# Kernel tuning notes

Hardware: AMD Instinct MI355X
Metric: run time of the kernel (lower is better)

Reference implementation:

```python
import jax, jax.numpy as jnp
import numpy as np

N_NODES = 50000
N_EDGES = 800000
D_IN = 100
HID = 128
N_LAYERS = 3
N_GRAPHS = 64


def setup_inputs() -> dict:
    key = jax.random.key(0)
    ks = jax.random.split(key, 10)
    x = jax.random.normal(ks[0], (N_NODES, D_IN), dtype=jnp.float32)
    edge_index = jax.random.randint(ks[1], (2, N_EDGES), 0, N_NODES, dtype=jnp.int64)
    batch = jnp.sort(jax.random.randint(ks[2], (N_NODES,), 0, N_GRAPHS, dtype=jnp.int64))
    s = 1.0 / np.sqrt(D_IN)
    W_enc = jax.random.uniform(ks[3], (D_IN, HID), jnp.float32, -s, s)
    b_enc = jax.random.uniform(ks[4], (HID,), jnp.float32, -s, s)
    sh = 1.0 / np.sqrt(HID)
    gcn_W = jax.random.uniform(ks[5], (N_LAYERS, HID, HID), jnp.float32, -sh, sh)
    gcn_b = jax.random.uniform(ks[6], (N_LAYERS, HID), jnp.float32, -sh, sh)
    W_reg = jax.random.uniform(ks[7], (HID, 1), jnp.float32, -sh, sh)
    b_reg = jax.random.uniform(ks[8], (1,), jnp.float32, -sh, sh)
    return {"x": x, "edge_index": edge_index, "batch": batch,
            "W_enc": W_enc, "b_enc": b_enc, "gcn_W": gcn_W, "gcn_b": gcn_b,
            "W_reg": W_reg, "b_reg": b_reg}


def reference(x, edge_index, batch, W_enc, b_enc, gcn_W, gcn_b, W_reg, b_reg):
    N = x.shape[0]
    # node encoder
    h = x @ W_enc + b_enc  # [N, HID]
    # GCN normalization with self-loops (edge_weight = 1, PyG gcn_norm)
    loop = jnp.arange(N, dtype=edge_index.dtype)
    src = jnp.concatenate([edge_index[0], loop])  # [E+N]
    dst = jnp.concatenate([edge_index[1], loop])
    deg = jax.ops.segment_sum(jnp.ones_like(src, dtype=h.dtype), dst, num_segments=N)
    dinv = jnp.where(deg > 0, jax.lax.rsqrt(deg), 0.0)
    norm = dinv[src] * dinv[dst]  # [E+N]
    for i in range(N_LAYERS):
        m = (h @ gcn_W[i])[src] * norm[:, None]           # gather + scale messages
        h = jax.ops.segment_sum(m, dst, num_segments=N)   # scatter-add aggregate
        h = jax.nn.relu(h + gcn_b[i])
    # global mean pool over graphs
    sums = jax.ops.segment_sum(h, batch, num_segments=N_GRAPHS)
    cnt = jax.ops.segment_sum(jnp.ones((N,), dtype=h.dtype), batch, num_segments=N_GRAPHS)
    pooled = sums / jnp.maximum(cnt, 1.0)[:, None]        # [N_GRAPHS, HID]
    return pooled @ W_reg + b_reg                         # [N_GRAPHS, 1]
```

## Files before the change

kernel.cpp:

```cpp
#include <hip/hip_runtime.h>
#include <hip/hip_fp16.h>

#define N_NODES 50000
#define N_EDGES 800000
#define D_INN 100
#define HID 128
#define N_GRAPHS 64
#define NBLK ((N_NODES + 255) / 256)
#define POOL_ROWS 128
#define POOL_BLOCKS ((N_NODES + POOL_ROWS - 1) / POOL_ROWS)

__global__ void k_init(int* __restrict__ deg, int* __restrict__ cnt,
                       float* __restrict__ sums) {
    int i = blockIdx.x * 256 + threadIdx.x;
    if (i < N_NODES) { deg[i] = 1; cnt[i] = 0; }
    if (i < N_GRAPHS * HID) sums[i] = 0.f;
}

__global__ void k_deg(const int* __restrict__ dst, int* __restrict__ deg) {
    int e = blockIdx.x * 256 + threadIdx.x;
    if (e < N_EDGES) atomicAdd(&deg[dst[e]], 1);
}

__global__ void k_dinv(const int* __restrict__ deg, float* __restrict__ dinv) {
    int i = blockIdx.x * 256 + threadIdx.x;
    if (i < N_NODES) dinv[i] = rsqrtf((float)deg[i]);
}

__global__ __launch_bounds__(256) void k_scan1(const int* __restrict__ deg,
                                               int* __restrict__ incl,
                                               int* __restrict__ bsums) {
    __shared__ int sm[256];
    int i = blockIdx.x * 256 + threadIdx.x;
    int v = (i < N_NODES) ? deg[i] : 0;
    sm[threadIdx.x] = v;
    __syncthreads();
    for (int off = 1; off < 256; off <<= 1) {
        int t = (threadIdx.x >= off) ? sm[threadIdx.x - off] : 0;
        __syncthreads();
        sm[threadIdx.x] += t;
        __syncthreads();
    }
    if (i < N_NODES) incl[i] = sm[threadIdx.x];
    if (threadIdx.x == 255) bsums[blockIdx.x] = sm[255];
}

__global__ __launch_bounds__(256) void k_scan2(const int* __restrict__ bsums,
                                               int* __restrict__ boff) {
    __shared__ int sm[256];
    int v = (threadIdx.x < NBLK) ? bsums[threadIdx.x] : 0;
    sm[threadIdx.x] = v;
    __syncthreads();
    for (int off = 1; off < 256; off <<= 1) {
        int t = (threadIdx.x >= off) ? sm[threadIdx.x - off] : 0;
        __syncthreads();
        sm[threadIdx.x] += t;
        __syncthreads();
    }
    boff[threadIdx.x] = sm[threadIdx.x] - v;
}

__global__ void k_scan3(const int* __restrict__ incl, const int* __restrict__ boff,
                        int* __restrict__ offsets) {
    int i = blockIdx.x * 256 + threadIdx.x;
    if (i < N_NODES) offsets[i + 1] = incl[i] + boff[blockIdx.x];
    if (i == 0) offsets[0] = 0;
}

__global__ void k_fill(const int* __restrict__ src, const int* __restrict__ dst,
                       const int* __restrict__ offsets, int* __restrict__ cnt,
                       int* __restrict__ csr_src) {
    int e = blockIdx.x * 256 + threadIdx.x;
    if (e < N_EDGES) {
        int s = src[e], d = dst[e];
        int pos = offsets[d] + atomicAdd(&cnt[d], 1);
        csr_src[pos] = s;
    } else if (e < N_EDGES + N_NODES) {
        int i = e - N_EDGES;
        int pos = offsets[i] + atomicAdd(&cnt[i], 1);
        csr_src[pos] = i;
    }
}

template <int K, bool BIAS, bool FOLD>
__global__ __launch_bounds__(256) void k_gemm(const float* __restrict__ in,
                                              const float* __restrict__ W,
                                              const float* __restrict__ bias,
                                              const float* __restrict__ dinv,
                                              void* __restrict__ outp) {
    __shared__ float lw[K * HID];
    __shared__ float lx[32 * K];
    for (int i = threadIdx.x; i < K * HID / 4; i += 256)
        ((float4*)lw)[i] = ((const float4*)W)[i];
    const int cq = threadIdx.x & 31;
    const int rg = threadIdx.x >> 5;
    float4 zero; zero.x = zero.y = zero.z = zero.w = 0.f;
    float4 bv = zero;
    if (BIAS) bv = ((const float4*)bias)[cq];
    const float4* lw4 = (const float4*)lw;
    float* outf = (float*)outp;
    __half* outh = (__half*)outp;
    const int nch = (N_NODES + 31) / 32;
    for (int c = blockIdx.x; c < nch; c += gridDim.x) {
        int r0 = c * 32;
        __syncthreads();
        for (int i = threadIdx.x; i < 32 * K / 4; i += 256) {
            int fi = i * 4;
            int rr = fi / K, kk = fi % K;
            int gr = r0 + rr;
            ((float4*)lx)[i] = (gr < N_NODES) ? *(const float4*)(in + gr * K + kk) : zero;
        }
        __syncthreads();
        float4 a0 = bv, a1 = bv, a2 = bv, a3 = bv;
#pragma unroll 8
        for (int k = 0; k < K; ++k) {
            float4 w = lw4[k * 32 + cq];
            float x0 = lx[(rg +  0) * K + k];
            float x1 = lx[(rg +  8) * K + k];
            float x2 = lx[(rg + 16) * K + k];
            float x3 = lx[(rg + 24) * K + k];
            a0.x = fmaf(x0, w.x, a0.x); a0.y = fmaf(x0, w.y, a0.y);
            a0.z = fmaf(x0, w.z, a0.z); a0.w = fmaf(x0, w.w, a0.w);
            a1.x = fmaf(x1, w.x, a1.x); a1.y = fmaf(x1, w.y, a1.y);
            a1.z = fmaf(x1, w.z, a1.z); a1.w = fmaf(x1, w.w, a1.w);
            a2.x = fmaf(x2, w.x, a2.x); a2.y = fmaf(x2, w.y, a2.y);
            a2.z = fmaf(x2, w.z, a2.z); a2.w = fmaf(x2, w.w, a2.w);
            a3.x = fmaf(x3, w.x, a3.x); a3.y = fmaf(x3, w.y, a3.y);
            a3.z = fmaf(x3, w.z, a3.z); a3.w = fmaf(x3, w.w, a3.w);
        }
        int gr = r0 + rg;
        if (FOLD) {
#pragma unroll
            for (int q = 0; q < 4; ++q) {
                int r = gr + q * 8;
                if (r < N_NODES) {
                    float4 a = (q == 0) ? a0 : (q == 1) ? a1 : (q == 2) ? a2 : a3;
                    float s = dinv[r];
                    ushort4 h;
                    h.x = __half_as_ushort(__float2half(a.x * s));
                    h.y = __half_as_ushort(__float2half(a.y * s));
                    h.z = __half_as_ushort(__float2half(a.z * s));
                    h.w = __half_as_ushort(__float2half(a.w * s));
                    *(ushort4*)(outh + r * HID + cq * 4) = h;
                }
            }
        } else {
            if (gr      < N_NODES) *(float4*)(outf + (gr     ) * HID + cq * 4) = a0;
            if (gr +  8 < N_NODES) *(float4*)(outf + (gr +  8) * HID + cq * 4) = a1;
            if (gr + 16 < N_NODES) *(float4*)(outf + (gr + 16) * HID + cq * 4) = a2;
            if (gr + 24 < N_NODES) *(float4*)(outf + (gr + 24) * HID + cq * 4) = a3;
        }
    }
}

__global__ __launch_bounds__(256) void k_agg(const __half* __restrict__ B,
                                             const int* __restrict__ offsets,
                                             const int* __restrict__ csr_src,
                                             const float* __restrict__ dinv,
                                             const float* __restrict__ bias,
                                             float* __restrict__ A) {
    int node = (blockIdx.x * 256 + threadIdx.x) >> 6;
    int lane = threadIdx.x & 63;
    if (node >= N_NODES) return;
    int beg = offsets[node], end = offsets[node + 1];
    float ax0 = 0.f, ay0 = 0.f, ax1 = 0.f, ay1 = 0.f;
    const __half2* B2 = (const __half2*)B;
    int j = beg;
    while (j < end) {
        int take = end - j; if (take > 64) take = 64;
        int s_l = (lane < take) ? csr_src[j + lane] : 0;
        int t = 0;
        for (; t + 4 <= take; t += 4) {
            int s0 = __shfl(s_l, t + 0), s1 = __shfl(s_l, t + 1);
            int s2 = __shfl(s_l, t + 2), s3 = __shfl(s_l, t + 3);
            __half2 v0 = B2[s0 * 64 + lane];
            __half2 v1 = B2[s1 * 64 + lane];
            __half2 v2 = B2[s2 * 64 + lane];
            __half2 v3 = B2[s3 * 64 + lane];
            float2 f0 = __half22float2(v0);
            float2 f1 = __half22float2(v1);
            float2 f2 = __half22float2(v2);
            float2 f3 = __half22float2(v3);
            ax0 += f0.x; ay0 += f0.y;
            ax1 += f1.x; ay1 += f1.y;
            ax0 += f2.x; ay0 += f2.y;
            ax1 += f3.x; ay1 += f3.y;
        }
        for (; t < take; ++t) {
            int s = __shfl(s_l, t);
            float2 f = __half22float2(B2[s * 64 + lane]);
            ax0 += f.x; ay0 += f.y;
        }
        j += take;
    }
    float dn = dinv[node];
    float2 b = ((const float2*)bias)[lane];
    float2 r;
    r.x = fmaxf(fmaf(dn, ax0 + ax1, b.x), 0.f);
    r.y = fmaxf(fmaf(dn, ay0 + ay1, b.y), 0.f);
    ((float2*)A)[node * 64 + lane] = r;
}

__global__ __launch_bounds__(128) void k_pool_part(const float* __restrict__ A,
                                                   const int* __restrict__ batch,
                                                   float* __restrict__ sums) {
    int base = blockIdx.x * POOL_ROWS;
    if (base >= N_NODES) return;
    int c = threadIdx.x;
    int end = base + POOL_ROWS;
    if (end > N_NODES) end = N_NODES;
    float acc = 0.f;
    int g = batch[base];
    for (int n = base; n < end; ++n) {
        int bg = batch[n];
        if (bg != g) {
            atomicAdd(&sums[g * HID + c], acc);
            acc = 0.f;
            g = bg;
        }
        acc += A[n * HID + c];
    }
    atomicAdd(&sums[g * HID + c], acc);
}

__global__ __launch_bounds__(128) void k_head(const float* __restrict__ sums,
                                              const int* __restrict__ batch,
                                              const float* __restrict__ W_reg,
                                              const float* __restrict__ b_reg,
                                              float* __restrict__ out) {
    int g = blockIdx.x;
    int lo = 0, hi = N_NODES;
    while (lo < hi) { int mid = (lo + hi) >> 1; if (batch[mid] < g) lo = mid + 1; else hi = mid; }
    int start = lo;
    hi = N_NODES;
    while (lo < hi) { int mid = (lo + hi) >> 1; if (batch[mid] < g + 1) lo = mid + 1; else hi = mid; }
    int end = lo;
    float cnt = (float)((end - start) > 0 ? (end - start) : 1);
    float v = (sums[g * HID + threadIdx.x] / cnt) * W_reg[threadIdx.x];
    for (int off = 32; off > 0; off >>= 1) v += __shfl_down(v, off);
    __shared__ float sm[2];
    if ((threadIdx.x & 63) == 0) sm[threadIdx.x >> 6] = v;
    __syncthreads();
    if (threadIdx.x == 0) out[g] = sm[0] + sm[1] + b_reg[0];
}

extern "C" void kernel_launch(void* const* d_in, const int* in_sizes, int n_in,
                              void* d_out, int out_size, void* d_ws, size_t ws_size,
                              hipStream_t stream) {
    const float* x      = (const float*)d_in[0];
    const int*   e_src  = (const int*)d_in[1];
    const int*   e_dst  = e_src + N_EDGES;
    const int*   batch  = (const int*)d_in[2];
    const float* W_enc  = (const float*)d_in[3];
    const float* b_enc  = (const float*)d_in[4];
    const float* gcn_W  = (const float*)d_in[5];
    const float* gcn_b  = (const float*)d_in[6];
    const float* W_reg  = (const float*)d_in[7];
    const float* b_reg  = (const float*)d_in[8];
    float* out = (float*)d_out;

    char* p = (char*)d_ws;
    auto carve = [&](size_t bytes) { char* q = p; p += (bytes + 255) & ~(size_t)255; return q; };
    float*  bufA    = (float*) carve(sizeof(float)  * N_NODES * HID);
    __half* bufB    = (__half*)carve(sizeof(__half) * N_NODES * HID);
    int*    csr_src = (int*)   carve(sizeof(int)    * (N_EDGES + N_NODES));
    int*    deg     = (int*)   carve(sizeof(int)    * N_NODES);
    int*    cnt     = (int*)   carve(sizeof(int)    * N_NODES);
    int*    offsets = (int*)   carve(sizeof(int)    * (N_NODES + 1));
    int*    incl    = (int*)   carve(sizeof(int)    * N_NODES);
    int*    bsums   = (int*)   carve(sizeof(int)    * 256);
    int*    boff    = (int*)   carve(sizeof(int)    * 256);
    float*  dinv    = (float*) carve(sizeof(float)  * N_NODES);
    float*  sums    = (float*) carve(sizeof(float)  * N_GRAPHS * HID);

    k_init<<<NBLK, 256, 0, stream>>>(deg, cnt, sums);
    k_deg<<<(N_EDGES + 255) / 256, 256, 0, stream>>>(e_dst, deg);
    k_dinv<<<NBLK, 256, 0, stream>>>(deg, dinv);
    k_scan1<<<NBLK, 256, 0, stream>>>(deg, incl, bsums);
    k_scan2<<<1, 256, 0, stream>>>(bsums, boff);
    k_scan3<<<NBLK, 256, 0, stream>>>(incl, boff, offsets);
    k_fill<<<(N_EDGES + N_NODES + 255) / 256, 256, 0, stream>>>(
        e_src, e_dst, offsets, cnt, csr_src);

    k_gemm<D_INN, true, false><<<512, 256, 0, stream>>>(x, W_enc, b_enc, nullptr, bufA);
    for (int l = 0; l < 3; ++l) {
        k_gemm<HID, false, true><<<512, 256, 0, stream>>>(
            bufA, gcn_W + l * HID * HID, nullptr, dinv, bufB);
        k_agg<<<(N_NODES * 64 + 255) / 256, 256, 0, stream>>>(
            bufB, offsets, csr_src, dinv, gcn_b + l * HID, bufA);
    }
    k_pool_part<<<POOL_BLOCKS, 128, 0, stream>>>(bufA, batch, sums);
    k_head<<<N_GRAPHS, 128, 0, stream>>>(sums, batch, W_reg, b_reg, out);
}
```

Before: 435.2 us.

## Use MFMA fp16 GEMMs, store activations in half, simplify CSR build

```diff
diff --git a/kernel.cpp b/kernel.cpp
--- a/kernel.cpp
+++ b/kernel.cpp
@@ -10,16 +10,24 @@
 #define POOL_ROWS 128
 #define POOL_BLOCKS ((N_NODES + POOL_ROWS - 1) / POOL_ROWS)
 
-__global__ void k_init(int* __restrict__ deg, int* __restrict__ cnt,
-                       float* __restrict__ sums) {
-    int i = blockIdx.x * 256 + threadIdx.x;
-    if (i < N_NODES) { deg[i] = 1; cnt[i] = 0; }
+typedef _Float16 f16x8 __attribute__((ext_vector_type(8)));
+typedef float f32x4 __attribute__((ext_vector_type(4)));
+
+__global__ void k_init(int* __restrict__ deg, float* __restrict__ sums) {
+    int i = blockIdx.x * 256 + threadIdx.x;
+    if (i < N_NODES) deg[i] = 1;
     if (i < N_GRAPHS * HID) sums[i] = 0.f;
 }
 
 __global__ void k_deg(const int* __restrict__ dst, int* __restrict__ deg) {
-    int e = blockIdx.x * 256 + threadIdx.x;
-    if (e < N_EDGES) atomicAdd(&deg[dst[e]], 1);
+    int t = blockIdx.x * 256 + threadIdx.x;
+    if (t < N_EDGES / 4) {
+        int4 d = ((const int4*)dst)[t];
+        atomicAdd(&deg[d.x], 1);
+        atomicAdd(&deg[d.y], 1);
+        atomicAdd(&deg[d.z], 1);
+        atomicAdd(&deg[d.w], 1);
+    }
 }
 
 __global__ void k_dinv(const int* __restrict__ deg, float* __restrict__ dinv) {
@@ -61,33 +69,46 @@
 }
 
 __global__ void k_scan3(const int* __restrict__ incl, const int* __restrict__ boff,
-                        int* __restrict__ offsets) {
-    int i = blockIdx.x * 256 + threadIdx.x;
-    if (i < N_NODES) offsets[i + 1] = incl[i] + boff[blockIdx.x];
+                        const int* __restrict__ deg, int* __restrict__ offsets,
+                        int* __restrict__ cursor, int* __restrict__ csr_src) {
+    int i = blockIdx.x * 256 + threadIdx.x;
+    if (i < N_NODES) {
+        int off1 = incl[i] + boff[blockIdx.x];
+        offsets[i + 1] = off1;
+        int p0 = off1 - deg[i];
+        csr_src[p0] = i;
+        cursor[i] = p0 + 1;
+    }
     if (i == 0) offsets[0] = 0;
 }
 
 __global__ void k_fill(const int* __restrict__ src, const int* __restrict__ dst,
-                       const int* __restrict__ offsets, int* __restrict__ cnt,
-                       int* __restrict__ csr_src) {
-    int e = blockIdx.x * 256 + threadIdx.x;
-    if (e < N_EDGES) {
-        int s = src[e], d = dst[e];
-        int pos = offsets[d] + atomicAdd(&cnt[d], 1);
-        csr_src[pos] = s;
-    } else if (e < N_EDGES + N_NODES) {
-        int i = e - N_EDGES;
-        int pos = offsets[i] + atomicAdd(&cnt[i], 1);
-        csr_src[pos] = i;
-    }
-}
-
-template <int K, bool BIAS, bool FOLD>
-__global__ __launch_bounds__(256) void k_gemm(const float* __restrict__ in,
-                                              const float* __restrict__ W,
-                                              const float* __restrict__ bias,
-                                              const float* __restrict__ dinv,
-                                              void* __restrict__ outp) {
+                       int* __restrict__ cursor, int* __restrict__ csr_src) {
+    int t = blockIdx.x * 256 + threadIdx.x;
+    if (t < N_EDGES / 2) {
+        int2 s = ((const int2*)src)[t];
+        int2 d = ((const int2*)dst)[t];
+        int p0 = atomicAdd(&cursor[d.x], 1);
+        csr_src[p0] = s.x;
+        int p1 = atomicAdd(&cursor[d.y], 1);
+        csr_src[p1] = s.y;
+    }
+}
+
+__global__ void k_wt(const float* __restrict__ W, __half* __restrict__ Wt) {
+    int i = blockIdx.x * 256 + threadIdx.x;
+    if (i < 3 * HID * HID) {
+        int l = i >> 14, rem = i & 16383;
+        int c = rem >> 7, k = rem & 127;
+        Wt[(l << 14) + c * HID + k] = __float2half(W[(l << 14) + k * HID + c]);
+    }
+}
+
+__global__ __launch_bounds__(256) void k_gemm_enc(const float* __restrict__ in,
+                                                  const float* __restrict__ W,
+                                                  const float* __restrict__ bias,
+                                                  __half* __restrict__ outh) {
+    const int K = D_INN;
     __shared__ float lw[K * HID];
     __shared__ float lx[32 * K];
     for (int i = threadIdx.x; i < K * HID / 4; i += 256)
@@ -95,11 +116,8 @@
     const int cq = threadIdx.x & 31;
     const int rg = threadIdx.x >> 5;
     float4 zero; zero.x = zero.y = zero.z = zero.w = 0.f;
-    float4 bv = zero;
-    if (BIAS) bv = ((const float4*)bias)[cq];
+    float4 bv = ((const float4*)bias)[cq];
     const float4* lw4 = (const float4*)lw;
-    float* outf = (float*)outp;
-    __half* outh = (__half*)outp;
     const int nch = (N_NODES + 31) / 32;
     for (int c = blockIdx.x; c < nch; c += gridDim.x) {
         int r0 = c * 32;
@@ -112,7 +130,7 @@
         }
         __syncthreads();
         float4 a0 = bv, a1 = bv, a2 = bv, a3 = bv;
-#pragma unroll 8
+#pragma unroll 4
         for (int k = 0; k < K; ++k) {
             float4 w = lw4[k * 32 + cq];
             float x0 = lx[(rg +  0) * K + k];
@@ -129,26 +147,61 @@
             a3.z = fmaf(x3, w.z, a3.z); a3.w = fmaf(x3, w.w, a3.w);
         }
         int gr = r0 + rg;
-        if (FOLD) {
 #pragma unroll
-            for (int q = 0; q < 4; ++q) {
-                int r = gr + q * 8;
-                if (r < N_NODES) {
-                    float4 a = (q == 0) ? a0 : (q == 1) ? a1 : (q == 2) ? a2 : a3;
-                    float s = dinv[r];
-                    ushort4 h;
-                    h.x = __half_as_ushort(__float2half(a.x * s));
-                    h.y = __half_as_ushort(__float2half(a.y * s));
-                    h.z = __half_as_ushort(__float2half(a.z * s));
-                    h.w = __half_as_ushort(__float2half(a.w * s));
-                    *(ushort4*)(outh + r * HID + cq * 4) = h;
-                }
+        for (int q = 0; q < 4; ++q) {
+            int r = gr + q * 8;
+            if (r < N_NODES) {
+                float4 a = (q == 0) ? a0 : (q == 1) ? a1 : (q == 2) ? a2 : a3;
+                ushort4 h;
+                h.x = __half_as_ushort(__float2half(a.x));
+                h.y = __half_as_ushort(__float2half(a.y));
+                h.z = __half_as_ushort(__float2half(a.z));
+                h.w = __half_as_ushort(__float2half(a.w));
+                *(ushort4*)(outh + r * HID + cq * 4) = h;
             }
-        } else {
-            if (gr      < N_NODES) *(float4*)(outf + (gr     ) * HID + cq * 4) = a0;
-            if (gr +  8 < N_NODES) *(float4*)(outf + (gr +  8) * HID + cq * 4) = a1;
-            if (gr + 16 < N_NODES) *(float4*)(outf + (gr + 16) * HID + cq * 4) = a2;
-            if (gr + 24 < N_NODES) *(float4*)(outf + (gr + 24) * HID + cq * 4) = a3;
+        }
+    }
+}
+
+__global__ __launch_bounds__(256) void k_gemm_mfma(const _Float16* __restrict__ A,
+                                                   const _Float16* __restrict__ Wt,
+                                                   const float* __restrict__ dinv,
+                                                   _Float16* __restrict__ out) {
+    const int lane = threadIdx.x & 63;
+    const int wave = threadIdx.x >> 6;
+    const int l15  = lane & 15;
+    const int lhi  = lane >> 4;
+    f16x8 bf0[4], bf1[4];
+#pragma unroll
+    for (int ks = 0; ks < 4; ++ks) {
+        int col0 = wave * 32 + l15;
+        int col1 = wave * 32 + 16 + l15;
+        bf0[ks] = *(const f16x8*)(Wt + col0 * HID + ks * 32 + lhi * 8);
+        bf1[ks] = *(const f16x8*)(Wt + col1 * HID + ks * 32 + lhi * 8);
+    }
+    for (int chunk = blockIdx.x; chunk < N_NODES / 16; chunk += gridDim.x) {
+        int row0 = chunk * 16;
+        const _Float16* Ar = A + (row0 + l15) * HID + lhi * 8;
+        f16x8 af0 = *(const f16x8*)(Ar);
+        f16x8 af1 = *(const f16x8*)(Ar + 32);
+        f16x8 af2 = *(const f16x8*)(Ar + 64);
+        f16x8 af3 = *(const f16x8*)(Ar + 96);
+        f32x4 acc0 = {0.f, 0.f, 0.f, 0.f};
+        f32x4 acc1 = {0.f, 0.f, 0.f, 0.f};
+        acc0 = __builtin_amdgcn_mfma_f32_16x16x32_f16(af0, bf0[0], acc0, 0, 0, 0);
+        acc1 = __builtin_amdgcn_mfma_f32_16x16x32_f16(af0, bf1[0], acc1, 0, 0, 0);
+        acc0 = __builtin_amdgcn_mfma_f32_16x16x32_f16(af1, bf0[1], acc0, 0, 0, 0);
+        acc1 = __builtin_amdgcn_mfma_f32_16x16x32_f16(af1, bf1[1], acc1, 0, 0, 0);
+        acc0 = __builtin_amdgcn_mfma_f32_16x16x32_f16(af2, bf0[2], acc0, 0, 0, 0);
+        acc1 = __builtin_amdgcn_mfma_f32_16x16x32_f16(af2, bf1[2], acc1, 0, 0, 0);
+        acc0 = __builtin_amdgcn_mfma_f32_16x16x32_f16(af3, bf0[3], acc0, 0, 0, 0);
+        acc1 = __builtin_amdgcn_mfma_f32_16x16x32_f16(af3, bf1[3], acc1, 0, 0, 0);
+#pragma unroll
+        for (int r = 0; r < 4; ++r) {
+            int row = row0 + lhi * 4 + r;
+            float dr = dinv[row];
+            out[row * HID + wave * 32 + l15]      = (_Float16)(acc0[r] * dr);
+            out[row * HID + wave * 32 + 16 + l15] = (_Float16)(acc1[r] * dr);
         }
     }
 }
@@ -158,7 +211,7 @@
                                              const int* __restrict__ csr_src,
                                              const float* __restrict__ dinv,
                                              const float* __restrict__ bias,
-                                             float* __restrict__ A) {
+                                             __half* __restrict__ A) {
     int node = (blockIdx.x * 256 + threadIdx.x) >> 6;
     int lane = threadIdx.x & 63;
     if (node >= N_NODES) return;
@@ -173,14 +226,10 @@
         for (; t + 4 <= take; t += 4) {
             int s0 = __shfl(s_l, t + 0), s1 = __shfl(s_l, t + 1);
             int s2 = __shfl(s_l, t + 2), s3 = __shfl(s_l, t + 3);
-            __half2 v0 = B2[s0 * 64 + lane];
-            __half2 v1 = B2[s1 * 64 + lane];
-            __half2 v2 = B2[s2 * 64 + lane];
-            __half2 v3 = B2[s3 * 64 + lane];
-            float2 f0 = __half22float2(v0);
-            float2 f1 = __half22float2(v1);
-            float2 f2 = __half22float2(v2);
-            float2 f3 = __half22float2(v3);
+            float2 f0 = __half22float2(B2[s0 * 64 + lane]);
+            float2 f1 = __half22float2(B2[s1 * 64 + lane]);
+            float2 f2 = __half22float2(B2[s2 * 64 + lane]);
+            float2 f3 = __half22float2(B2[s3 * 64 + lane]);
             ax0 += f0.x; ay0 += f0.y;
             ax1 += f1.x; ay1 += f1.y;
             ax0 += f2.x; ay0 += f2.y;
@@ -195,32 +244,35 @@
     }
     float dn = dinv[node];
     float2 b = ((const float2*)bias)[lane];
-    float2 r;
-    r.x = fmaxf(fmaf(dn, ax0 + ax1, b.x), 0.f);
-    r.y = fmaxf(fmaf(dn, ay0 + ay1, b.y), 0.f);
-    ((float2*)A)[node * 64 + lane] = r;
-}
-
-__global__ __launch_bounds__(128) void k_pool_part(const float* __restrict__ A,
-                                                   const int* __restrict__ batch,
-                                                   float* __restrict__ sums) {
+    float rx = fmaxf(fmaf(dn, ax0 + ax1, b.x), 0.f);
+    float ry = fmaxf(fmaf(dn, ay0 + ay1, b.y), 0.f);
+    ((__half2*)A)[node * 64 + lane] = __floats2half2_rn(rx, ry);
+}
+
+__global__ __launch_bounds__(64) void k_pool_part(const __half* __restrict__ A,
+                                                  const int* __restrict__ batch,
+                                                  float* __restrict__ sums) {
     int base = blockIdx.x * POOL_ROWS;
     if (base >= N_NODES) return;
     int c = threadIdx.x;
     int end = base + POOL_ROWS;
     if (end > N_NODES) end = N_NODES;
-    float acc = 0.f;
+    const __half2* A2 = (const __half2*)A;
+    float ax = 0.f, ay = 0.f;
     int g = batch[base];
     for (int n = base; n < end; ++n) {
         int bg = batch[n];
         if (bg != g) {
-            atomicAdd(&sums[g * HID + c], acc);
-            acc = 0.f;
+            atomicAdd(&sums[g * HID + 2 * c], ax);
+            atomicAdd(&sums[g * HID + 2 * c + 1], ay);
+            ax = 0.f; ay = 0.f;
             g = bg;
         }
-        acc += A[n * HID + c];
-    }
-    atomicAdd(&sums[g * HID + c], acc);
+        float2 f = __half22float2(A2[n * 64 + c]);
+        ax += f.x; ay += f.y;
+    }
+    atomicAdd(&sums[g * HID + 2 * c], ax);
+    atomicAdd(&sums[g * HID + 2 * c + 1], ay);
 }
 
 __global__ __launch_bounds__(128) void k_head(const float* __restrict__ sums,
@@ -261,11 +313,12 @@
 
     char* p = (char*)d_ws;
     auto carve = [&](size_t bytes) { char* q = p; p += (bytes + 255) & ~(size_t)255; return q; };
-    float*  bufA    = (float*) carve(sizeof(float)  * N_NODES * HID);
-    __half* bufB    = (__half*)carve(sizeof(__half) * N_NODES * HID);
+    __half* hA      = (__half*)carve(sizeof(__half) * N_NODES * HID);
+    __half* msg     = (__half*)carve(sizeof(__half) * N_NODES * HID);
+    __half* Wt      = (__half*)carve(sizeof(__half) * 3 * HID * HID);
     int*    csr_src = (int*)   carve(sizeof(int)    * (N_EDGES + N_NODES));
     int*    deg     = (int*)   carve(sizeof(int)    * N_NODES);
-    int*    cnt     = (int*)   carve(sizeof(int)    * N_NODES);
+    int*    cursor  = (int*)   carve(sizeof(int)    * N_NODES);
     int*    offsets = (int*)   carve(sizeof(int)    * (N_NODES + 1));
     int*    incl    = (int*)   carve(sizeof(int)    * N_NODES);
     int*    bsums   = (int*)   carve(sizeof(int)    * 256);
@@ -273,22 +326,23 @@
     float*  dinv    = (float*) carve(sizeof(float)  * N_NODES);
     float*  sums    = (float*) carve(sizeof(float)  * N_GRAPHS * HID);
 
-    k_init<<<NBLK, 256, 0, stream>>>(deg, cnt, sums);
-    k_deg<<<(N_EDGES + 255) / 256, 256, 0, stream>>>(e_dst, deg);
+    k_init<<<NBLK, 256, 0, stream>>>(deg, sums);
+    k_deg<<<(N_EDGES / 4 + 255) / 256, 256, 0, stream>>>(e_dst, deg);
     k_dinv<<<NBLK, 256, 0, stream>>>(deg, dinv);
     k_scan1<<<NBLK, 256, 0, stream>>>(deg, incl, bsums);
     k_scan2<<<1, 256, 0, stream>>>(bsums, boff);
-    k_scan3<<<NBLK, 256, 0, stream>>>(incl, boff, offsets);
-    k_fill<<<(N_EDGES + N_NODES + 255) / 256, 256, 0, stream>>>(
-        e_src, e_dst, offsets, cnt, csr_src);
-
-    k_gemm<D_INN, true, false><<<512, 256, 0, stream>>>(x, W_enc, b_enc, nullptr, bufA);
+    k_scan3<<<NBLK, 256, 0, stream>>>(incl, boff, deg, offsets, cursor, csr_src);
+    k_fill<<<(N_EDGES / 2 + 255) / 256, 256, 0, stream>>>(e_src, e_dst, cursor, csr_src);
+    k_wt<<<(3 * HID * HID + 255) / 256, 256, 0, stream>>>(gcn_W, Wt);
+
+    k_gemm_enc<<<512, 256, 0, stream>>>(x, W_enc, b_enc, hA);
     for (int l = 0; l < 3; ++l) {
-        k_gemm<HID, false, true><<<512, 256, 0, stream>>>(
-            bufA, gcn_W + l * HID * HID, nullptr, dinv, bufB);
+        k_gemm_mfma<<<640, 256, 0, stream>>>(
+            (const _Float16*)hA, (const _Float16*)(Wt + l * HID * HID), dinv,
+            (_Float16*)msg);
         k_agg<<<(N_NODES * 64 + 255) / 256, 256, 0, stream>>>(
-            bufB, offsets, csr_src, dinv, gcn_b + l * HID, bufA);
-    }
-    k_pool_part<<<POOL_BLOCKS, 128, 0, stream>>>(bufA, batch, sums);
+            msg, offsets, csr_src, dinv, gcn_b + l * HID, hA);
+    }
+    k_pool_part<<<POOL_BLOCKS, 64, 0, stream>>>(hA, batch, sums);
     k_head<<<N_GRAPHS, 128, 0, stream>>>(sums, batch, W_reg, b_reg, out);
 }
```

New measurement: 401.6 us. -7.7%, faster.
